# Performance work log

Measured on AMD Instinct MI355X. Metric: run time of the kernel, lower is better.

## Reference

```python
import jax, jax.numpy as jnp
import numpy as np

B, T, D_IN, D_LAT, N_UNITS = 2048, 200, 64, 64, 100


def setup_inputs() -> dict:
    key = jax.random.key(0)
    ks = jax.random.split(key, 20)
    s = 0.05
    inp = {
        "data": jax.random.normal(ks[0], (B, T, D_IN), dtype=jnp.float32),
        "time_steps": jnp.arange(T, dtype=jnp.float32),
        # ODE func: 2-layer MLP latent -> n_units -> latent (tanh hidden)
        "Wf1": jax.random.normal(ks[1], (D_LAT, N_UNITS), jnp.float32) * s,
        "bf1": jnp.zeros((N_UNITS,), jnp.float32),
        "Wf2": jax.random.normal(ks[2], (N_UNITS, D_LAT), jnp.float32) * s,
        "bf2": jnp.zeros((D_LAT,), jnp.float32),
        # GRU update gate net: [latent+input] -> n_units -> latent
        "Wz1": jax.random.normal(ks[3], (D_LAT + D_IN, N_UNITS), jnp.float32) * s,
        "bz1": jnp.zeros((N_UNITS,), jnp.float32),
        "Wz2": jax.random.normal(ks[4], (N_UNITS, D_LAT), jnp.float32) * s,
        "bz2": jnp.zeros((D_LAT,), jnp.float32),
        # GRU reset gate net
        "Wr1": jax.random.normal(ks[5], (D_LAT + D_IN, N_UNITS), jnp.float32) * s,
        "br1": jnp.zeros((N_UNITS,), jnp.float32),
        "Wr2": jax.random.normal(ks[6], (N_UNITS, D_LAT), jnp.float32) * s,
        "br2": jnp.zeros((D_LAT,), jnp.float32),
        # GRU candidate-state net
        "Wh1": jax.random.normal(ks[7], (D_LAT + D_IN, N_UNITS), jnp.float32) * s,
        "bh1": jnp.zeros((N_UNITS,), jnp.float32),
        "Wh2": jax.random.normal(ks[8], (N_UNITS, D_LAT), jnp.float32) * s,
        "bh2": jnp.zeros((D_LAT,), jnp.float32),
    }
    return inp


def _mlp(x, W1, b1, W2, b2):
    return jnp.tanh(x @ W1 + b1) @ W2 + b2


def reference(data, time_steps, Wf1, bf1, Wf2, bf2,
              Wz1, bz1, Wz2, bz2, Wr1, br1, Wr2, br2,
              Wh1, bh1, Wh2, bh2):
    n_traj = data.shape[0]
    latent_dim = Wf1.shape[0]
    prev_y0 = jnp.zeros((n_traj, latent_dim), dtype=data.dtype)

    # Faithful to original control flow: with uniform arange time steps,
    # |prev_t - t_i| < minimum_step always holds -> single explicit Euler step.
    # Original code swaps (prev_t, t_i) at the end of each iteration, so the
    # effective dt at iteration i is: i==1 -> ts[1]-ts[0]; i>=2 -> ts[i-2]-ts[i-1].
    dts = jnp.concatenate([time_steps[1:2] - time_steps[0:1],
                           time_steps[:-2] - time_steps[1:-1]])  # [T-1]

    xs_data = jnp.moveaxis(data[:, 1:, :], 0, 1)  # [T-1, B, D_in]

    def step(prev_y, inp):
        x, dt = inp
        # Euler step of the neural ODE
        yi_ode = prev_y + _mlp(prev_y, Wf1, bf1, Wf2, bf2) * dt
        # GRU update (GRUUnitOriginal): gates from concat(y_ode, x)
        c = jnp.concatenate([yi_ode, x], axis=-1)
        z = jax.nn.sigmoid(_mlp(c, Wz1, bz1, Wz2, bz2))
        r = jax.nn.sigmoid(_mlp(c, Wr1, br1, Wr2, br2))
        ch = jnp.concatenate([yi_ode * r, x], axis=-1)
        h = jnp.tanh(_mlp(ch, Wh1, bh1, Wh2, bh2))
        y = (1.0 - z) * h + z * yi_ode
        return y, y

    yi, ys = jax.lax.scan(step, prev_y0, (xs_data, dts))
    latent_ys = jnp.moveaxis(ys, 0, 1)  # [B, T-1, latent]
    return yi, latent_ys
```

## Files before the change

### kernel.cpp

```cpp
#include <hip/hip_runtime.h>


#define NBT   2048
#define TSTEP 200
#define NT    8

typedef short s8v __attribute__((ext_vector_type(8)));
typedef float f4v __attribute__((ext_vector_type(4)));

#define RB_Y 144
#define RB_C 272
#define OFF_Y  0
#define OFF_C  2304
#define OFF_HF 6656
#define OFF_HZ 11008
#define OFF_HR 15360
#define OFF_HH 19712
#define SMEM_TOT 24064

__device__ __forceinline__ unsigned short f2bf(float f) {
    unsigned int b = __float_as_uint(f);
    return (unsigned short)((b + 0x7fffu + ((b >> 16) & 1u)) >> 16);
}
__device__ __forceinline__ float tanh_f(float x) {
    float e = __expf(2.0f * x);
    return fmaf(-2.0f, __builtin_amdgcn_rcpf(e + 1.0f), 1.0f);
}
__device__ __forceinline__ float sigm_f(float x) {
    return __builtin_amdgcn_rcpf(1.0f + __expf(-x));
}

__device__ __forceinline__ f4v mfma16(s8v a, s8v b, f4v c) {
    return __builtin_amdgcn_mfma_f32_16x16x32_bf16(a, b, c, 0, 0, 0);
}

__device__ __forceinline__ s8v load_bfrag(const float* __restrict__ W,
                                          int Ncols, int Krows, int k0, int n) {
    s8v r;
#pragma unroll
    for (int j = 0; j < 8; ++j) {
        const int k = k0 + j;
        const float v = (k < Krows && n < Ncols) ? W[k * Ncols + n] : 0.0f;
        r[j] = (short)f2bf(v);
    }
    return r;
}

template <int RB>
__device__ __forceinline__ s8v load_af(const char* base, int lane, int kt) {
    return *(const s8v*)(base + (lane & 15) * RB + ((lane >> 4) * 16) + kt * 64);
}

__device__ __forceinline__ void store_tanh(char* base, int n0, int lane, f4v a) {
#pragma unroll
    for (int r = 0; r < 4; ++r) {
        const int row = (lane >> 4) * 4 + r;
        *(short*)(base + row * RB_C + (n0 + (lane & 15)) * 2) =
            f2bf(tanh_f(a[r]));
    }
}

__device__ __forceinline__ f4v splat(float b) { f4v v = {b, b, b, b}; return v; }

__global__ __launch_bounds__(256, 1) void ode_rnn_mfma(
    const float* __restrict__ data, const float* __restrict__ tsv,
    const float* __restrict__ Wf1, const float* __restrict__ bf1,
    const float* __restrict__ Wf2, const float* __restrict__ bf2,
    const float* __restrict__ Wz1, const float* __restrict__ bz1,
    const float* __restrict__ Wz2, const float* __restrict__ bz2,
    const float* __restrict__ Wr1, const float* __restrict__ br1,
    const float* __restrict__ Wr2, const float* __restrict__ br2,
    const float* __restrict__ Wh1, const float* __restrict__ bh1,
    const float* __restrict__ Wh2, const float* __restrict__ bh2,
    float* __restrict__ out_yi, float* __restrict__ out_ys)
{
    __shared__ __align__(16) char smem[SMEM_TOT];

    const int tid  = threadIdx.x;
    const int lane = tid & 63;
    const int wv   = tid >> 6;
    const int b0   = blockIdx.x * NT;

    for (int i = tid; i < SMEM_TOT / 4; i += 256) ((unsigned*)smem)[i] = 0u;

    const int kb  = (lane >> 4) * 8;
    const int nA  = wv * 16 + (lane & 15);
    const int nB  = (wv + 4) * 16 + (lane & 15);
    const int n2  = wv * 16 + (lane & 15);

    s8v Bf1[2][2], Bz1[2][4], Br1[2][4], Bh1[2][4];
    s8v Bf2[4], Bz2[4], Br2[4], Bh2[4];
#pragma unroll
    for (int kt = 0; kt < 2; ++kt) {
        Bf1[0][kt] = load_bfrag(Wf1, 100, 64, kt * 32 + kb, nA);
        Bf1[1][kt] = load_bfrag(Wf1, 100, 64, kt * 32 + kb, nB);
    }
#pragma unroll
    for (int kt = 0; kt < 4; ++kt) {
        Bz1[0][kt] = load_bfrag(Wz1, 100, 128, kt * 32 + kb, nA);
        Bz1[1][kt] = load_bfrag(Wz1, 100, 128, kt * 32 + kb, nB);
        Br1[0][kt] = load_bfrag(Wr1, 100, 128, kt * 32 + kb, nA);
        Br1[1][kt] = load_bfrag(Wr1, 100, 128, kt * 32 + kb, nB);
        Bh1[0][kt] = load_bfrag(Wh1, 100, 128, kt * 32 + kb, nA);
        Bh1[1][kt] = load_bfrag(Wh1, 100, 128, kt * 32 + kb, nB);
        Bf2[kt] = load_bfrag(Wf2, 64, 100, kt * 32 + kb, n2);
        Bz2[kt] = load_bfrag(Wz2, 64, 100, kt * 32 + kb, n2);
        Br2[kt] = load_bfrag(Wr2, 64, 100, kt * 32 + kb, n2);
        Bh2[kt] = load_bfrag(Wh2, 64, 100, kt * 32 + kb, n2);
    }

    const float bf1A = (nA < 100) ? bf1[nA] : 0.0f;
    const float bf1B = (nB < 100) ? bf1[nB] : 0.0f;
    const float bz1A = (nA < 100) ? bz1[nA] : 0.0f;
    const float bz1B = (nB < 100) ? bz1[nB] : 0.0f;
    const float br1A = (nA < 100) ? br1[nA] : 0.0f;
    const float br1B = (nB < 100) ? br1[nB] : 0.0f;
    const float bh1A = (nA < 100) ? bh1[nA] : 0.0f;
    const float bh1B = (nB < 100) ? bh1[nB] : 0.0f;
    const float bF2 = bf2[n2], bZ2 = bz2[n2], bR2 = br2[n2], bH2 = bh2[n2];

    const int xtr = tid >> 5;
    const int xd  = (tid & 31) * 2;

    f4v y_reg = splat(0.0f);
    __syncthreads();

    for (int s = 0; s < TSTEP - 1; ++s) {
        const float2 xv = *(const float2*)
            &data[((size_t)(b0 + xtr) * TSTEP + (s + 1)) * 64 + xd];
        const float dt = (s == 0) ? (tsv[1] - tsv[0]) : (tsv[s - 1] - tsv[s]);

        {
            const s8v ya0 = load_af<RB_Y>(smem + OFF_Y, lane, 0);
            const s8v ya1 = load_af<RB_Y>(smem + OFF_Y, lane, 1);
            f4v aA = splat(bf1A), aB = splat(bf1B);
            aA = mfma16(ya0, Bf1[0][0], aA); aA = mfma16(ya1, Bf1[0][1], aA);
            aB = mfma16(ya0, Bf1[1][0], aB); aB = mfma16(ya1, Bf1[1][1], aB);
            store_tanh(smem + OFF_HF, wv * 16, lane, aA);
            store_tanh(smem + OFF_HF, (wv + 4) * 16, lane, aB);
        }
        __syncthreads();

        f4v yode;
        {
            f4v ac = splat(bF2);
#pragma unroll
            for (int kt = 0; kt < 4; ++kt)
                ac = mfma16(load_af<RB_C>(smem + OFF_HF, lane, kt), Bf2[kt], ac);
#pragma unroll
            for (int r = 0; r < 4; ++r) yode[r] = fmaf(dt, ac[r], y_reg[r]);
#pragma unroll
            for (int r = 0; r < 4; ++r) {
                const int row = (lane >> 4) * 4 + r;
                *(short*)(smem + OFF_C + row * RB_C + n2 * 2) = f2bf(yode[r]);
            }
            const unsigned xp = (unsigned)f2bf(xv.x) | ((unsigned)f2bf(xv.y) << 16);
            *(unsigned*)(smem + OFF_C + xtr * RB_C + 128 + (tid & 31) * 4) = xp;
        }
        __syncthreads();

        {
            s8v c0 = load_af<RB_C>(smem + OFF_C, lane, 0);
            s8v c1 = load_af<RB_C>(smem + OFF_C, lane, 1);
            s8v c2 = load_af<RB_C>(smem + OFF_C, lane, 2);
            s8v c3 = load_af<RB_C>(smem + OFF_C, lane, 3);
            f4v az0 = splat(bz1A), az1 = splat(bz1B);
            f4v ar0 = splat(br1A), ar1 = splat(br1B);
            az0 = mfma16(c0, Bz1[0][0], az0); az0 = mfma16(c1, Bz1[0][1], az0);
            az0 = mfma16(c2, Bz1[0][2], az0); az0 = mfma16(c3, Bz1[0][3], az0);
            az1 = mfma16(c0, Bz1[1][0], az1); az1 = mfma16(c1, Bz1[1][1], az1);
            az1 = mfma16(c2, Bz1[1][2], az1); az1 = mfma16(c3, Bz1[1][3], az1);
            ar0 = mfma16(c0, Br1[0][0], ar0); ar0 = mfma16(c1, Br1[0][1], ar0);
            ar0 = mfma16(c2, Br1[0][2], ar0); ar0 = mfma16(c3, Br1[0][3], ar0);
            ar1 = mfma16(c0, Br1[1][0], ar1); ar1 = mfma16(c1, Br1[1][1], ar1);
            ar1 = mfma16(c2, Br1[1][2], ar1); ar1 = mfma16(c3, Br1[1][3], ar1);
            store_tanh(smem + OFF_HZ, wv * 16, lane, az0);
            store_tanh(smem + OFF_HZ, (wv + 4) * 16, lane, az1);
            store_tanh(smem + OFF_HR, wv * 16, lane, ar0);
            store_tanh(smem + OFF_HR, (wv + 4) * 16, lane, ar1);
        }
        __syncthreads();

        f4v zf;
        {
            f4v az = splat(bZ2), ar = splat(bR2);
#pragma unroll
            for (int kt = 0; kt < 4; ++kt) {
                az = mfma16(load_af<RB_C>(smem + OFF_HZ, lane, kt), Bz2[kt], az);
                ar = mfma16(load_af<RB_C>(smem + OFF_HR, lane, kt), Br2[kt], ar);
            }
#pragma unroll
            for (int r = 0; r < 4; ++r) {
                zf[r] = sigm_f(az[r]);
                const float rr = sigm_f(ar[r]);
                const int row = (lane >> 4) * 4 + r;
                *(short*)(smem + OFF_C + row * RB_C + n2 * 2) =
                    f2bf(yode[r] * rr);
            }
        }
        __syncthreads();

        {
            s8v d0 = load_af<RB_C>(smem + OFF_C, lane, 0);
            s8v d1 = load_af<RB_C>(smem + OFF_C, lane, 1);
            s8v d2 = load_af<RB_C>(smem + OFF_C, lane, 2);
            s8v d3 = load_af<RB_C>(smem + OFF_C, lane, 3);
            f4v ah0 = splat(bh1A), ah1 = splat(bh1B);
            ah0 = mfma16(d0, Bh1[0][0], ah0); ah0 = mfma16(d1, Bh1[0][1], ah0);
            ah0 = mfma16(d2, Bh1[0][2], ah0); ah0 = mfma16(d3, Bh1[0][3], ah0);
            ah1 = mfma16(d0, Bh1[1][0], ah1); ah1 = mfma16(d1, Bh1[1][1], ah1);
            ah1 = mfma16(d2, Bh1[1][2], ah1); ah1 = mfma16(d3, Bh1[1][3], ah1);
            store_tanh(smem + OFF_HH, wv * 16, lane, ah0);
            store_tanh(smem + OFF_HH, (wv + 4) * 16, lane, ah1);
        }
        __syncthreads();

        {
            f4v ah = splat(bH2);
#pragma unroll
            for (int kt = 0; kt < 4; ++kt)
                ah = mfma16(load_af<RB_C>(smem + OFF_HH, lane, kt), Bh2[kt], ah);
#pragma unroll
            for (int r = 0; r < 4; ++r) {
                const float h = tanh_f(ah[r]);
                y_reg[r] = (1.0f - zf[r]) * h + zf[r] * yode[r];
                const int row = (lane >> 4) * 4 + r;
                *(short*)(smem + OFF_Y + row * RB_Y + n2 * 2) = f2bf(y_reg[r]);
            }
            if (lane < 32) {
#pragma unroll
                for (int r = 0; r < 4; ++r) {
                    const int row = (lane >> 4) * 4 + r;
                    out_ys[((size_t)(b0 + row) * (TSTEP - 1) + s) * 64 + n2] =
                        y_reg[r];
                }
                if (s == TSTEP - 2) {
#pragma unroll
                    for (int r = 0; r < 4; ++r) {
                        const int row = (lane >> 4) * 4 + r;
                        out_yi[(size_t)(b0 + row) * 64 + n2] = y_reg[r];
                    }
                }
            }
        }
        __syncthreads();
    }
}

extern "C" void kernel_launch(void* const* d_in, const int* in_sizes, int n_in,
                              void* d_out, int out_size, void* d_ws, size_t ws_size,
                              hipStream_t stream) {
    const float* data = (const float*)d_in[0];
    const float* tsv  = (const float*)d_in[1];
    const float* Wf1 = (const float*)d_in[2];  const float* bf1 = (const float*)d_in[3];
    const float* Wf2 = (const float*)d_in[4];  const float* bf2 = (const float*)d_in[5];
    const float* Wz1 = (const float*)d_in[6];  const float* bz1 = (const float*)d_in[7];
    const float* Wz2 = (const float*)d_in[8];  const float* bz2 = (const float*)d_in[9];
    const float* Wr1 = (const float*)d_in[10]; const float* br1 = (const float*)d_in[11];
    const float* Wr2 = (const float*)d_in[12]; const float* br2 = (const float*)d_in[13];
    const float* Wh1 = (const float*)d_in[14]; const float* bh1 = (const float*)d_in[15];
    const float* Wh2 = (const float*)d_in[16]; const float* bh2 = (const float*)d_in[17];

    float* out_yi = (float*)d_out;
    float* out_ys = out_yi + (size_t)NBT * 64;

    ode_rnn_mfma<<<NBT / NT, 256, 0, stream>>>(
        data, tsv, Wf1, bf1, Wf2, bf2, Wz1, bz1, Wz2, bz2,
        Wr1, br1, Wr2, br2, Wh1, bh1, Wh2, bh2, out_yi, out_ys);
}
```

Measured before the change: 420.4 us.

## Split block work across eight waves with role-specialised wave groups

The block grows from 4 to 8 waves. Each wave now computes one 16-column tile of the hidden layers instead of two. The second-layer matmuls are split so that waves 0-3 handle the ODE output, update gate and candidate, while waves 4-7 handle the reset gate and the input load. Float-to-bf16 conversions switch to the packed hardware instruction. This is meant to shorten each wave's serial chain per timestep and allow two blocks per CU, at the cost of more barrier participants and an extra LDS read-back of yode on the reset path.

After: 355.5 us. 1.18x faster.

```diff
diff --git a/kernel.cpp b/kernel.cpp
--- a/kernel.cpp
+++ b/kernel.cpp
@@ -18,10 +18,18 @@
 #define OFF_HH 19712
 #define SMEM_TOT 24064
 
+__device__ __forceinline__ unsigned cvtpk(float lo, float hi) {
+    unsigned r;
+    asm("v_cvt_pk_bf16_f32 %0, %1, %2" : "=v"(r) : "v"(lo), "v"(hi));
+    return r;
+}
 __device__ __forceinline__ unsigned short f2bf(float f) {
     unsigned int b = __float_as_uint(f);
     return (unsigned short)((b + 0x7fffu + ((b >> 16) & 1u)) >> 16);
 }
+__device__ __forceinline__ float bf2f(unsigned short u) {
+    return __uint_as_float(((unsigned)u) << 16);
+}
 __device__ __forceinline__ float tanh_f(float x) {
     float e = __expf(2.0f * x);
     return fmaf(-2.0f, __builtin_amdgcn_rcpf(e + 1.0f), 1.0f);
@@ -29,10 +37,10 @@
 __device__ __forceinline__ float sigm_f(float x) {
     return __builtin_amdgcn_rcpf(1.0f + __expf(-x));
 }
-
 __device__ __forceinline__ f4v mfma16(s8v a, s8v b, f4v c) {
     return __builtin_amdgcn_mfma_f32_16x16x32_bf16(a, b, c, 0, 0, 0);
 }
+__device__ __forceinline__ f4v splat(float b) { f4v v = {b, b, b, b}; return v; }
 
 __device__ __forceinline__ s8v load_bfrag(const float* __restrict__ W,
                                           int Ncols, int Krows, int k0, int n) {
@@ -51,18 +59,20 @@
     return *(const s8v*)(base + (lane & 15) * RB + ((lane >> 4) * 16) + kt * 64);
 }
 
+__device__ __forceinline__ void store4(char* base, int col2, int rb, int pitch,
+                                       float v0, float v1, float v2, float v3) {
+    const unsigned u01 = cvtpk(v0, v1), u23 = cvtpk(v2, v3);
+    *(short*)(base + (rb + 0) * pitch + col2) = (short)(u01 & 0xffffu);
+    *(short*)(base + (rb + 1) * pitch + col2) = (short)(u01 >> 16);
+    *(short*)(base + (rb + 2) * pitch + col2) = (short)(u23 & 0xffffu);
+    *(short*)(base + (rb + 3) * pitch + col2) = (short)(u23 >> 16);
+}
 __device__ __forceinline__ void store_tanh(char* base, int n0, int lane, f4v a) {
-#pragma unroll
-    for (int r = 0; r < 4; ++r) {
-        const int row = (lane >> 4) * 4 + r;
-        *(short*)(base + row * RB_C + (n0 + (lane & 15)) * 2) =
-            f2bf(tanh_f(a[r]));
-    }
-}
-
-__device__ __forceinline__ f4v splat(float b) { f4v v = {b, b, b, b}; return v; }
-
-__global__ __launch_bounds__(256, 1) void ode_rnn_mfma(
+    store4(base, (n0 + (lane & 15)) * 2, (lane >> 4) * 4, RB_C,
+           tanh_f(a[0]), tanh_f(a[1]), tanh_f(a[2]), tanh_f(a[3]));
+}
+
+__global__ __launch_bounds__(512, 2) void ode_rnn_mfma8(
     const float* __restrict__ data, const float* __restrict__ tsv,
     const float* __restrict__ Wf1, const float* __restrict__ bf1,
     const float* __restrict__ Wf2, const float* __restrict__ bf2,
@@ -79,143 +89,139 @@
     const int tid  = threadIdx.x;
     const int lane = tid & 63;
     const int wv   = tid >> 6;
+    const bool isA = (wv < 4);
     const int b0   = blockIdx.x * NT;
 
-    for (int i = tid; i < SMEM_TOT / 4; i += 256) ((unsigned*)smem)[i] = 0u;
-
-    const int kb  = (lane >> 4) * 8;
-    const int nA  = wv * 16 + (lane & 15);
-    const int nB  = (wv + 4) * 16 + (lane & 15);
-    const int n2  = wv * 16 + (lane & 15);
-
-    s8v Bf1[2][2], Bz1[2][4], Br1[2][4], Bh1[2][4];
-    s8v Bf2[4], Bz2[4], Br2[4], Bh2[4];
-#pragma unroll
-    for (int kt = 0; kt < 2; ++kt) {
-        Bf1[0][kt] = load_bfrag(Wf1, 100, 64, kt * 32 + kb, nA);
-        Bf1[1][kt] = load_bfrag(Wf1, 100, 64, kt * 32 + kb, nB);
-    }
+    for (int i = tid; i < SMEM_TOT / 4; i += 512) ((unsigned*)smem)[i] = 0u;
+
+    const int kb = (lane >> 4) * 8;
+    const int n1 = wv * 16 + (lane & 15);
+    const int n2 = (wv & 3) * 16 + (lane & 15);
+
+    s8v Bf1[2], Bz1[4], Br1[4], Bh1[4];
+    s8v Bf2[4], Bz2[4], Bh2[4], Br2[4];
+#pragma unroll
+    for (int kt = 0; kt < 2; ++kt)
+        Bf1[kt] = load_bfrag(Wf1, 100, 64, kt * 32 + kb, n1);
 #pragma unroll
     for (int kt = 0; kt < 4; ++kt) {
-        Bz1[0][kt] = load_bfrag(Wz1, 100, 128, kt * 32 + kb, nA);
-        Bz1[1][kt] = load_bfrag(Wz1, 100, 128, kt * 32 + kb, nB);
-        Br1[0][kt] = load_bfrag(Wr1, 100, 128, kt * 32 + kb, nA);
-        Br1[1][kt] = load_bfrag(Wr1, 100, 128, kt * 32 + kb, nB);
-        Bh1[0][kt] = load_bfrag(Wh1, 100, 128, kt * 32 + kb, nA);
-        Bh1[1][kt] = load_bfrag(Wh1, 100, 128, kt * 32 + kb, nB);
-        Bf2[kt] = load_bfrag(Wf2, 64, 100, kt * 32 + kb, n2);
-        Bz2[kt] = load_bfrag(Wz2, 64, 100, kt * 32 + kb, n2);
-        Br2[kt] = load_bfrag(Wr2, 64, 100, kt * 32 + kb, n2);
-        Bh2[kt] = load_bfrag(Wh2, 64, 100, kt * 32 + kb, n2);
-    }
-
-    const float bf1A = (nA < 100) ? bf1[nA] : 0.0f;
-    const float bf1B = (nB < 100) ? bf1[nB] : 0.0f;
-    const float bz1A = (nA < 100) ? bz1[nA] : 0.0f;
-    const float bz1B = (nB < 100) ? bz1[nB] : 0.0f;
-    const float br1A = (nA < 100) ? br1[nA] : 0.0f;
-    const float br1B = (nB < 100) ? br1[nB] : 0.0f;
-    const float bh1A = (nA < 100) ? bh1[nA] : 0.0f;
-    const float bh1B = (nB < 100) ? bh1[nB] : 0.0f;
-    const float bF2 = bf2[n2], bZ2 = bz2[n2], bR2 = br2[n2], bH2 = bh2[n2];
-
-    const int xtr = tid >> 5;
-    const int xd  = (tid & 31) * 2;
-
-    f4v y_reg = splat(0.0f);
+        Bz1[kt] = load_bfrag(Wz1, 100, 128, kt * 32 + kb, n1);
+        Br1[kt] = load_bfrag(Wr1, 100, 128, kt * 32 + kb, n1);
+        Bh1[kt] = load_bfrag(Wh1, 100, 128, kt * 32 + kb, n1);
+    }
+    if (isA) {
+#pragma unroll
+        for (int kt = 0; kt < 4; ++kt) {
+            Bf2[kt] = load_bfrag(Wf2, 64, 100, kt * 32 + kb, n2);
+            Bz2[kt] = load_bfrag(Wz2, 64, 100, kt * 32 + kb, n2);
+            Bh2[kt] = load_bfrag(Wh2, 64, 100, kt * 32 + kb, n2);
+        }
+    } else {
+#pragma unroll
+        for (int kt = 0; kt < 4; ++kt)
+            Br2[kt] = load_bfrag(Wr2, 64, 100, kt * 32 + kb, n2);
+    }
+
+    const float b1f = (n1 < 100) ? bf1[n1] : 0.0f;
+    const float b1z = (n1 < 100) ? bz1[n1] : 0.0f;
+    const float b1r = (n1 < 100) ? br1[n1] : 0.0f;
+    const float b1h = (n1 < 100) ? bh1[n1] : 0.0f;
+    const float bF2 = isA ? bf2[n2] : 0.0f;
+    const float bZ2 = isA ? bz2[n2] : 0.0f;
+    const float bH2 = isA ? bh2[n2] : 0.0f;
+    const float bR2 = isA ? 0.0f : br2[n2];
+
+    const int t2  = tid & 255;
+    const int xtr = t2 >> 5;
+    const int xd  = (t2 & 31) * 2;
+
+    const int col2 = n2 * 2;
+    const int rb   = (lane >> 4) * 4;
+
+    f4v y_reg = splat(0.0f), yode = splat(0.0f), zf = splat(0.0f);
     __syncthreads();
 
     for (int s = 0; s < TSTEP - 1; ++s) {
-        const float2 xv = *(const float2*)
-            &data[((size_t)(b0 + xtr) * TSTEP + (s + 1)) * 64 + xd];
+        float2 xv;
+        if (!isA)
+            xv = *(const float2*)&data[((size_t)(b0 + xtr) * TSTEP + (s + 1)) * 64 + xd];
         const float dt = (s == 0) ? (tsv[1] - tsv[0]) : (tsv[s - 1] - tsv[s]);
 
         {
             const s8v ya0 = load_af<RB_Y>(smem + OFF_Y, lane, 0);
             const s8v ya1 = load_af<RB_Y>(smem + OFF_Y, lane, 1);
-            f4v aA = splat(bf1A), aB = splat(bf1B);
-            aA = mfma16(ya0, Bf1[0][0], aA); aA = mfma16(ya1, Bf1[0][1], aA);
-            aB = mfma16(ya0, Bf1[1][0], aB); aB = mfma16(ya1, Bf1[1][1], aB);
-            store_tanh(smem + OFF_HF, wv * 16, lane, aA);
-            store_tanh(smem + OFF_HF, (wv + 4) * 16, lane, aB);
-        }
-        __syncthreads();
-
-        f4v yode;
+            f4v a = splat(b1f);
+            a = mfma16(ya0, Bf1[0], a);
+            a = mfma16(ya1, Bf1[1], a);
+            store_tanh(smem + OFF_HF, wv * 16, lane, a);
+        }
+        __syncthreads();
+
+        if (isA) {
+            f4v ac = splat(bF2);
+#pragma unroll
+            for (int kt = 0; kt < 4; ++kt)
+                ac = mfma16(load_af<RB_C>(smem + OFF_HF, lane, kt), Bf2[kt], ac);
+#pragma unroll
+            for (int r = 0; r < 4; ++r) yode[r] = fmaf(dt, ac[r], y_reg[r]);
+            store4(smem + OFF_C, col2, rb, RB_C, yode[0], yode[1], yode[2], yode[3]);
+        } else {
+            *(unsigned*)(smem + OFF_C + xtr * RB_C + 128 + (t2 & 31) * 4) =
+                cvtpk(xv.x, xv.y);
+        }
+        __syncthreads();
+
         {
-            f4v ac = splat(bF2);
-#pragma unroll
-            for (int kt = 0; kt < 4; ++kt)
-                ac = mfma16(load_af<RB_C>(smem + OFF_HF, lane, kt), Bf2[kt], ac);
-#pragma unroll
-            for (int r = 0; r < 4; ++r) yode[r] = fmaf(dt, ac[r], y_reg[r]);
+            const s8v c0 = load_af<RB_C>(smem + OFF_C, lane, 0);
+            const s8v c1 = load_af<RB_C>(smem + OFF_C, lane, 1);
+            const s8v c2 = load_af<RB_C>(smem + OFF_C, lane, 2);
+            const s8v c3 = load_af<RB_C>(smem + OFF_C, lane, 3);
+            f4v az = splat(b1z), ar = splat(b1r);
+            az = mfma16(c0, Bz1[0], az); az = mfma16(c1, Bz1[1], az);
+            az = mfma16(c2, Bz1[2], az); az = mfma16(c3, Bz1[3], az);
+            ar = mfma16(c0, Br1[0], ar); ar = mfma16(c1, Br1[1], ar);
+            ar = mfma16(c2, Br1[2], ar); ar = mfma16(c3, Br1[3], ar);
+            store_tanh(smem + OFF_HZ, wv * 16, lane, az);
+            store_tanh(smem + OFF_HR, wv * 16, lane, ar);
+        }
+        __syncthreads();
+
+        if (isA) {
+            f4v az = splat(bZ2);
+#pragma unroll
+            for (int kt = 0; kt < 4; ++kt)
+                az = mfma16(load_af<RB_C>(smem + OFF_HZ, lane, kt), Bz2[kt], az);
+#pragma unroll
+            for (int r = 0; r < 4; ++r) zf[r] = sigm_f(az[r]);
+        } else {
+            f4v ar = splat(bR2);
+#pragma unroll
+            for (int kt = 0; kt < 4; ++kt)
+                ar = mfma16(load_af<RB_C>(smem + OFF_HR, lane, kt), Br2[kt], ar);
+            float ch[4];
 #pragma unroll
             for (int r = 0; r < 4; ++r) {
-                const int row = (lane >> 4) * 4 + r;
-                *(short*)(smem + OFF_C + row * RB_C + n2 * 2) = f2bf(yode[r]);
+                const unsigned short yv =
+                    *(const unsigned short*)(smem + OFF_C + (rb + r) * RB_C + col2);
+                ch[r] = bf2f(yv) * sigm_f(ar[r]);
             }
-            const unsigned xp = (unsigned)f2bf(xv.x) | ((unsigned)f2bf(xv.y) << 16);
-            *(unsigned*)(smem + OFF_C + xtr * RB_C + 128 + (tid & 31) * 4) = xp;
+            store4(smem + OFF_C, col2, rb, RB_C, ch[0], ch[1], ch[2], ch[3]);
         }
         __syncthreads();
 
         {
-            s8v c0 = load_af<RB_C>(smem + OFF_C, lane, 0);
-            s8v c1 = load_af<RB_C>(smem + OFF_C, lane, 1);
-            s8v c2 = load_af<RB_C>(smem + OFF_C, lane, 2);
-            s8v c3 = load_af<RB_C>(smem + OFF_C, lane, 3);
-            f4v az0 = splat(bz1A), az1 = splat(bz1B);
-            f4v ar0 = splat(br1A), ar1 = splat(br1B);
-            az0 = mfma16(c0, Bz1[0][0], az0); az0 = mfma16(c1, Bz1[0][1], az0);
-            az0 = mfma16(c2, Bz1[0][2], az0); az0 = mfma16(c3, Bz1[0][3], az0);
-            az1 = mfma16(c0, Bz1[1][0], az1); az1 = mfma16(c1, Bz1[1][1], az1);
-            az1 = mfma16(c2, Bz1[1][2], az1); az1 = mfma16(c3, Bz1[1][3], az1);
-            ar0 = mfma16(c0, Br1[0][0], ar0); ar0 = mfma16(c1, Br1[0][1], ar0);
-            ar0 = mfma16(c2, Br1[0][2], ar0); ar0 = mfma16(c3, Br1[0][3], ar0);
-            ar1 = mfma16(c0, Br1[1][0], ar1); ar1 = mfma16(c1, Br1[1][1], ar1);
-            ar1 = mfma16(c2, Br1[1][2], ar1); ar1 = mfma16(c3, Br1[1][3], ar1);
-            store_tanh(smem + OFF_HZ, wv * 16, lane, az0);
-            store_tanh(smem + OFF_HZ, (wv + 4) * 16, lane, az1);
-            store_tanh(smem + OFF_HR, wv * 16, lane, ar0);
-            store_tanh(smem + OFF_HR, (wv + 4) * 16, lane, ar1);
-        }
-        __syncthreads();
-
-        f4v zf;
-        {
-            f4v az = splat(bZ2), ar = splat(bR2);
-#pragma unroll
-            for (int kt = 0; kt < 4; ++kt) {
-                az = mfma16(load_af<RB_C>(smem + OFF_HZ, lane, kt), Bz2[kt], az);
-                ar = mfma16(load_af<RB_C>(smem + OFF_HR, lane, kt), Br2[kt], ar);
-            }
-#pragma unroll
-            for (int r = 0; r < 4; ++r) {
-                zf[r] = sigm_f(az[r]);
-                const float rr = sigm_f(ar[r]);
-                const int row = (lane >> 4) * 4 + r;
-                *(short*)(smem + OFF_C + row * RB_C + n2 * 2) =
-                    f2bf(yode[r] * rr);
-            }
-        }
-        __syncthreads();
-
-        {
-            s8v d0 = load_af<RB_C>(smem + OFF_C, lane, 0);
-            s8v d1 = load_af<RB_C>(smem + OFF_C, lane, 1);
-            s8v d2 = load_af<RB_C>(smem + OFF_C, lane, 2);
-            s8v d3 = load_af<RB_C>(smem + OFF_C, lane, 3);
-            f4v ah0 = splat(bh1A), ah1 = splat(bh1B);
-            ah0 = mfma16(d0, Bh1[0][0], ah0); ah0 = mfma16(d1, Bh1[0][1], ah0);
-            ah0 = mfma16(d2, Bh1[0][2], ah0); ah0 = mfma16(d3, Bh1[0][3], ah0);
-            ah1 = mfma16(d0, Bh1[1][0], ah1); ah1 = mfma16(d1, Bh1[1][1], ah1);
-            ah1 = mfma16(d2, Bh1[1][2], ah1); ah1 = mfma16(d3, Bh1[1][3], ah1);
-            store_tanh(smem + OFF_HH, wv * 16, lane, ah0);
-            store_tanh(smem + OFF_HH, (wv + 4) * 16, lane, ah1);
-        }
-        __syncthreads();
-
-        {
+            const s8v d0 = load_af<RB_C>(smem + OFF_C, lane, 0);
+            const s8v d1 = load_af<RB_C>(smem + OFF_C, lane, 1);
+            const s8v d2 = load_af<RB_C>(smem + OFF_C, lane, 2);
+            const s8v d3 = load_af<RB_C>(smem + OFF_C, lane, 3);
+            f4v ah = splat(b1h);
+            ah = mfma16(d0, Bh1[0], ah); ah = mfma16(d1, Bh1[1], ah);
+            ah = mfma16(d2, Bh1[2], ah); ah = mfma16(d3, Bh1[3], ah);
+            store_tanh(smem + OFF_HH, wv * 16, lane, ah);
+        }
+        __syncthreads();
+
+        if (isA) {
             f4v ah = splat(bH2);
 #pragma unroll
             for (int kt = 0; kt < 4; ++kt)
@@ -224,22 +230,18 @@
             for (int r = 0; r < 4; ++r) {
                 const float h = tanh_f(ah[r]);
                 y_reg[r] = (1.0f - zf[r]) * h + zf[r] * yode[r];
-                const int row = (lane >> 4) * 4 + r;
-                *(short*)(smem + OFF_Y + row * RB_Y + n2 * 2) = f2bf(y_reg[r]);
             }
+            store4(smem + OFF_Y, col2, rb, RB_Y, y_reg[0], y_reg[1], y_reg[2], y_reg[3]);
             if (lane < 32) {
 #pragma unroll
                 for (int r = 0; r < 4; ++r) {
-                    const int row = (lane >> 4) * 4 + r;
-                    out_ys[((size_t)(b0 + row) * (TSTEP - 1) + s) * 64 + n2] =
-                        y_reg[r];
+                    const int row = rb + r;
+                    out_ys[((size_t)(b0 + row) * (TSTEP - 1) + s) * 64 + n2] = y_reg[r];
                 }
                 if (s == TSTEP - 2) {
 #pragma unroll
-                    for (int r = 0; r < 4; ++r) {
-                        const int row = (lane >> 4) * 4 + r;
-                        out_yi[(size_t)(b0 + row) * 64 + n2] = y_reg[r];
-                    }
+                    for (int r = 0; r < 4; ++r)
+                        out_yi[(size_t)(b0 + rb + r) * 64 + n2] = y_reg[r];
                 }
             }
         }
@@ -264,7 +266,7 @@
     float* out_yi = (float*)d_out;
     float* out_ys = out_yi + (size_t)NBT * 64;
 
-    ode_rnn_mfma<<<NBT / NT, 256, 0, stream>>>(
+    ode_rnn_mfma8<<<NBT / NT, 512, 0, stream>>>(
         data, tsv, Wf1, bf1, Wf2, bf2, Wz1, bz1, Wz2, bz2,
         Wr1, br1, Wr2, br2, Wh1, bh1, Wh2, bh2, out_yi, out_ys);
 }
```
